# Performance work log

Measured on AMD Instinct MI355X. Metric: run time of the kernel, lower is better.

## Reference

```python
import jax, jax.numpy as jnp
import numpy as np

HIDDEN = 1024
N_HEADS = 16
HEAD_DIM = HIDDEN // N_HEADS  # 64
SCALE = HEAD_DIM ** -0.5
B, QL, KVL = 2, 2048, 4096


def setup_inputs() -> dict:
    key = jax.random.key(0)
    ks = jax.random.split(key, 7)
    s = 0.02
    return {
        "query_states": jax.random.normal(ks[0], (B, QL, HIDDEN), jnp.float32),
        "key_states": jax.random.normal(ks[1], (B, KVL, HIDDEN), jnp.float32),
        "value_states": jax.random.normal(ks[2], (B, KVL, HIDDEN), jnp.float32),
        # torch nn.Linear weights: shape [out, in], applied as x @ W.T
        "Wq": jax.random.normal(ks[3], (HIDDEN, HIDDEN), jnp.float32) * s,
        "Wk": jax.random.normal(ks[4], (HIDDEN, HIDDEN), jnp.float32) * s,
        "Wv": jax.random.normal(ks[5], (HIDDEN, HIDDEN), jnp.float32) * s,
        "Wo": jax.random.normal(ks[6], (HIDDEN, HIDDEN), jnp.float32) * s,
    }


def reference(query_states, key_states, value_states, Wq, Wk, Wv, Wo):
    b, ql, _ = query_states.shape
    kvl = key_states.shape[1]
    # projections (torch Linear: x @ W.T)
    q = query_states @ Wq.T  # [b, ql, H]
    k = key_states @ Wk.T    # [b, kvl, H]
    v = value_states @ Wv.T  # [b, kvl, H]
    # split heads -> [b, h, s, d]
    q = q.reshape(b, ql, N_HEADS, HEAD_DIM).transpose(0, 2, 1, 3)
    k = k.reshape(b, kvl, N_HEADS, HEAD_DIM).transpose(0, 2, 1, 3)
    v = v.reshape(b, kvl, N_HEADS, HEAD_DIM).transpose(0, 2, 1, 3)
    # scores [b, h, ql, kvl]
    scores = jnp.einsum("bhqd,bhkd->bhqk", q, k) * SCALE
    attn = jax.nn.softmax(scores, axis=-1)
    out = jnp.einsum("bhqk,bhkd->bhqd", attn, v)  # [b, h, ql, d]
    out = out.transpose(0, 2, 1, 3).reshape(b, ql, HIDDEN)
    return out @ Wo.T
```

## Files before the change

### kernel.cpp

```cpp
#include <hip/hip_runtime.h>

#define HID   1024
#define NH    16
#define HD    64
#define QL    2048
#define KVL   4096
#define NB    2
#define QSCALE 0.180336880111120426f

typedef short s8v  __attribute__((ext_vector_type(8)));
typedef short s4v  __attribute__((ext_vector_type(4)));
typedef float f4v  __attribute__((ext_vector_type(4)));
typedef float f16x __attribute__((ext_vector_type(16)));

__device__ __forceinline__ unsigned short f2bf(float f) {
  unsigned int u = __builtin_bit_cast(unsigned int, f);
  u += 0x7FFFu + ((u >> 16) & 1u);
  return (unsigned short)(u >> 16);
}
__device__ __forceinline__ float bf2f(unsigned short h) {
  unsigned int u = ((unsigned int)h) << 16;
  return __builtin_bit_cast(float, u);
}
__device__ __forceinline__ float fexp2(float x) {
#if __has_builtin(__builtin_amdgcn_exp2f)
  return __builtin_amdgcn_exp2f(x);
#else
  return exp2f(x);
#endif
}

__device__ __forceinline__ unsigned truncpk(float lo, float hi) {
  unsigned ulo = __builtin_bit_cast(unsigned, lo);
  unsigned uhi = __builtin_bit_cast(unsigned, hi);
  return (ulo >> 16) | (uhi & 0xFFFF0000u);
}

__global__ __launch_bounds__(256)
void cast_all(const float* __restrict__ q, const float* __restrict__ k,
              const float* __restrict__ v, const float* __restrict__ wq,
              const float* __restrict__ wk, const float* __restrict__ wv,
              const float* __restrict__ wo, unsigned short* __restrict__ dst) {
  size_t c = (size_t)blockIdx.x * 256 + threadIdx.x;
  const float* src; size_t lc; float sc = 1.0f;
  if (c < 524288)       { src = q;  lc = c; }
  else if (c < 1572864) { src = k;  lc = c - 524288; }
  else if (c < 2621440) { src = v;  lc = c - 1572864; }
  else if (c < 2752512) { src = wq; lc = c - 2621440; sc = QSCALE; }
  else if (c < 2883584) { src = wk; lc = c - 2752512; }
  else if (c < 3014656) { src = wv; lc = c - 2883584; }
  else                  { src = wo; lc = c - 3014656; }
  const float4* p = (const float4*)(src + lc * 8);
  float4 a = p[0], b = p[1];
  union { s8v v8; unsigned short h[8]; } u;
  u.h[0] = f2bf(a.x * sc); u.h[1] = f2bf(a.y * sc);
  u.h[2] = f2bf(a.z * sc); u.h[3] = f2bf(a.w * sc);
  u.h[4] = f2bf(b.x * sc); u.h[5] = f2bf(b.y * sc);
  u.h[6] = f2bf(b.z * sc); u.h[7] = f2bf(b.w * sc);
  *(s8v*)(dst + c * 8) = u.v8;
}

typedef const __attribute__((address_space(1))) unsigned int* gas_t;
typedef __attribute__((address_space(3))) unsigned int*       las_t;

__device__ __forceinline__ void gl_lds16(const unsigned short* g, unsigned short* l) {
  __builtin_amdgcn_global_load_lds((gas_t)(const void*)g, (las_t)(void*)l, 16, 0, 0);
}

template <bool OUT_BF16>
__device__ __forceinline__ void gemm_body(const unsigned short* __restrict__ A,
                                          const unsigned short* __restrict__ B,
                                          void* __restrict__ Cv, int N, int K,
                                          int bx, int by,
                                          unsigned short (*As)[128 * 32],
                                          unsigned short (*Bs)[128 * 32]) {
  const int tid  = threadIdx.x;
  const int wave = tid >> 6, lane = tid & 63;
  const int wm = wave >> 1, wn = wave & 1;
  const int quad = lane >> 4, l15 = lane & 15;
  const int row0 = by * 128;
  const int col0 = bx * 128;
  const int srow = lane >> 2;
  const int scol = (lane & 3) * 8;

  f4v acc[4][4] = {};

#define G_STAGE(KI, BI)                                                         \
  {                                                                             \
    _Pragma("unroll")                                                           \
    for (int cc = 0; cc < 2; cc++) {                                            \
      int c = wave + cc * 4;                                                    \
      gl_lds16(A + (size_t)(row0 + c * 16 + srow) * K + (KI) * 32 + scol,       \
               &As[BI][c * 512]);                                               \
      gl_lds16(B + (size_t)(col0 + c * 16 + srow) * K + (KI) * 32 + scol,       \
               &Bs[BI][c * 512]);                                               \
    }                                                                           \
  }

  const int nk = K >> 5;
  G_STAGE(0, 0);
  __syncthreads();

  for (int ki = 0; ki < nk; ki++) {
    const int cur = ki & 1;
    if (ki + 1 < nk) G_STAGE(ki + 1, 1 - cur);

    s8v af[4], bf[4];
#pragma unroll
    for (int i = 0; i < 4; i++)
      af[i] = *(const s8v*)&As[cur][(wm * 64 + i * 16 + l15) * 32 + quad * 8];
#pragma unroll
    for (int j = 0; j < 4; j++)
      bf[j] = *(const s8v*)&Bs[cur][(wn * 64 + j * 16 + l15) * 32 + quad * 8];
#pragma unroll
    for (int i = 0; i < 4; i++)
#pragma unroll
      for (int j = 0; j < 4; j++)
        acc[i][j] = __builtin_amdgcn_mfma_f32_16x16x32_bf16(af[i], bf[j],
                                                            acc[i][j], 0, 0, 0);
    __syncthreads();
  }
#undef G_STAGE

#pragma unroll
  for (int i = 0; i < 4; i++) {
#pragma unroll
    for (int j = 0; j < 4; j++) {
      int r = row0 + wm * 64 + i * 16 + quad * 4;
      int c = col0 + wn * 64 + j * 16 + l15;
#pragma unroll
      for (int reg = 0; reg < 4; reg++) {
        float v = acc[i][j][reg];
        if constexpr (OUT_BF16)
          ((unsigned short*)Cv)[(size_t)(r + reg) * N + c] = f2bf(v);
        else
          ((float*)Cv)[(size_t)(r + reg) * N + c] = v;
      }
    }
  }
}

__global__ __launch_bounds__(256, 4)
void proj_fused(const unsigned short* __restrict__ qc, const unsigned short* __restrict__ kc,
                const unsigned short* __restrict__ vc, const unsigned short* __restrict__ wqc,
                const unsigned short* __restrict__ wkc, const unsigned short* __restrict__ wvc,
                unsigned short* __restrict__ qp, unsigned short* __restrict__ kp,
                unsigned short* __restrict__ vpt) {
  __shared__ unsigned short As[2][128 * 32];
  __shared__ unsigned short Bs[2][128 * 32];
  int bid = blockIdx.x;
  if (bid < 256) {
    gemm_body<true>(qc, wqc, qp, HID, HID, bid & 7, bid >> 3, As, Bs);
  } else if (bid < 768) {
    int l = bid - 256;
    gemm_body<true>(kc, wkc, kp, HID, HID, l & 7, l >> 3, As, Bs);
  } else {
    int l = bid - 768;
    int b = l >> 8, r = l & 255;
    gemm_body<true>(wvc, vc + (size_t)b * KVL * HID,
                    vpt + (size_t)b * HID * KVL, KVL, HID, r & 31, r >> 5, As, Bs);
  }
}

__global__ __launch_bounds__(256, 4)
void o_gemm(const unsigned short* __restrict__ ao, const unsigned short* __restrict__ woc,
            float* __restrict__ out) {
  __shared__ unsigned short As[2][128 * 32];
  __shared__ unsigned short Bs[2][128 * 32];
  int bid = blockIdx.x;
  gemm_body<false>(ao, woc, out, HID, HID, bid & 7, bid >> 3, As, Bs);
}

#define LDSK 40

template <typename T>
__device__ __forceinline__ void stage_tile(unsigned short* dst, const T* src,
                                           int ld, int tid, float sc) {
#pragma unroll
  for (int rep = 0; rep < 2; rep++) {
    int s = rep * 256 + tid;
    int row = s >> 2;
    int cs  = (s & 3) * 8;
    const T* p = src + (size_t)row * ld + cs;
    s8v val;
    if constexpr (sizeof(T) == 4) {
      float4 f0 = *(const float4*)p;
      float4 f1 = *(const float4*)(p + 4);
      union { s8v v; unsigned short h[8]; } u;
      u.h[0] = f2bf(f0.x * sc); u.h[1] = f2bf(f0.y * sc);
      u.h[2] = f2bf(f0.z * sc); u.h[3] = f2bf(f0.w * sc);
      u.h[4] = f2bf(f1.x * sc); u.h[5] = f2bf(f1.y * sc);
      u.h[6] = f2bf(f1.z * sc); u.h[7] = f2bf(f1.w * sc);
      val = u.v;
    } else {
      val = *(const s8v*)p;
    }
    *(s8v*)&dst[row * LDSK + cs] = val;
  }
}

template <typename TA, typename TB, bool OUT_BF16>
__global__ __launch_bounds__(256)
void gemm_conv(const TA* __restrict__ A, const TB* __restrict__ B,
               void* __restrict__ Cv, int M, int N, int K, float bscale,
               long long bz, long long cz) {
  __shared__ unsigned short As[128 * LDSK];
  __shared__ unsigned short Bs[128 * LDSK];
  const TB* Bp = B + (size_t)blockIdx.z * (size_t)bz;
  const int tid  = threadIdx.x;
  const int wave = tid >> 6, lane = tid & 63;
  const int wm = wave >> 1, wn = wave & 1;
  const int quad = lane >> 4, l15 = lane & 15;
  const int row0 = blockIdx.y * 128;
  const int col0 = blockIdx.x * 128;

  f4v acc[4][4] = {};

  for (int k0 = 0; k0 < K; k0 += 32) {
    __syncthreads();
    stage_tile(As, A + (size_t)row0 * K + k0, K, tid, 1.0f);
    stage_tile(Bs, Bp + (size_t)col0 * K + k0, K, tid, bscale);
    __syncthreads();

    s8v af[4], bf[4];
#pragma unroll
    for (int i = 0; i < 4; i++)
      af[i] = *(const s8v*)&As[(wm * 64 + i * 16 + l15) * LDSK + quad * 8];
#pragma unroll
    for (int j = 0; j < 4; j++)
      bf[j] = *(const s8v*)&Bs[(wn * 64 + j * 16 + l15) * LDSK + quad * 8];
#pragma unroll
    for (int i = 0; i < 4; i++)
#pragma unroll
      for (int j = 0; j < 4; j++)
        acc[i][j] = __builtin_amdgcn_mfma_f32_16x16x32_bf16(af[i], bf[j],
                                                            acc[i][j], 0, 0, 0);
  }

  char* Cp = (char*)Cv + (size_t)blockIdx.z * (size_t)cz * (OUT_BF16 ? 2 : 4);
#pragma unroll
  for (int i = 0; i < 4; i++) {
#pragma unroll
    for (int j = 0; j < 4; j++) {
      int r = row0 + wm * 64 + i * 16 + quad * 4;
      int c = col0 + wn * 64 + j * 16 + l15;
#pragma unroll
      for (int reg = 0; reg < 4; reg++) {
        float v = acc[i][j][reg];
        if constexpr (OUT_BF16)
          ((unsigned short*)Cp)[(size_t)(r + reg) * N + c] = f2bf(v);
        else
          ((float*)Cp)[(size_t)(r + reg) * N + c] = v;
      }
    }
  }
}

template <bool SPLIT>
__global__ __launch_bounds__(256, 2)
void attn11(const unsigned short* __restrict__ qp,
            const unsigned short* __restrict__ kp,
            const unsigned short* __restrict__ vpt,
            unsigned short* __restrict__ po,
            float* __restrict__ pl,
            unsigned short* __restrict__ ao) {
  __shared__ unsigned short Ks[2][64 * 64];
  __shared__ unsigned short Vt[2][64 * 64];

  const int bid  = blockIdx.x;
  const int qb   = bid & 7;
  const int h    = (bid >> 3) & 15;
  const int b    = (bid >> 7) & 1;
  const int half = SPLIT ? (bid >> 8) : 0;
  const int tid  = threadIdx.x;
  const int wave = tid >> 6, lane = tid & 63;
  const int l31  = lane & 31, hi = lane >> 5;
  const int q0   = qb * 256 + wave * 64;
  const int kvoff = half * (KVL / 2);
  const int NT   = SPLIT ? (KVL / 128) : (KVL / 64);

  const unsigned short* kbase = kp + (size_t)b * KVL * HID + h * HD + (size_t)kvoff * HID;
  const unsigned short* vbase = vpt + (size_t)(b * NH + h) * HD * KVL + kvoff;

  int prow[2], pcol[2], pbase[2];
#pragma unroll
  for (int i = 0; i < 2; i++) {
    int p = (i * 4 + wave) * 64 + lane;
    prow[i]  = p >> 3;
    pcol[i]  = ((p & 7) ^ (prow[i] & 7)) * 8;
    pbase[i] = (i * 4 + wave) * 512;
  }

  s8v qf[2][4];
#pragma unroll
  for (int nt = 0; nt < 2; nt++) {
    const unsigned short* qrow = qp + (size_t)(b * QL + q0 + nt * 32 + l31) * HID + h * HD;
#pragma unroll
    for (int ks = 0; ks < 4; ks++)
      qf[nt][ks] = *(const s8v*)(qrow + ks * 16 + hi * 8);
  }

  union { unsigned w[4]; s8v v; } uones;
#pragma unroll
  for (int i = 0; i < 4; i++) uones.w[i] = 0x3F803F80u;

  f16x oacc[2][2] = {};
  f16x lacc[2]    = {};

#define STAGE_KV(KT, BI)                                                        \
  {                                                                             \
    const unsigned short* kb = kbase + (size_t)((KT) * 64) * HID;               \
    const unsigned short* vb = vbase + (KT) * 64;                               \
    _Pragma("unroll")                                                           \
    for (int i = 0; i < 2; i++) {                                               \
      gl_lds16(kb + (size_t)prow[i] * HID + pcol[i], &Ks[BI][pbase[i]]);        \
      gl_lds16(vb + (size_t)prow[i] * KVL + pcol[i], &Vt[BI][pbase[i]]);        \
    }                                                                           \
  }

  STAGE_KV(0, 0);
  __syncthreads();

  for (int kt = 0; kt < NT; kt++) {
    const int cur = kt & 1;
    if (kt + 1 < NT) STAGE_KV(kt + 1, 1 - cur);

    f16x sacc[2][2] = {};
    __builtin_amdgcn_s_setprio(1);
#pragma unroll
    for (int ks = 0; ks < 4; ks++)
#pragma unroll
      for (int mt = 0; mt < 2; mt++) {
        int row = mt * 32 + l31;
        int xc  = ((ks * 2 + hi) ^ (row & 7)) * 8;
        s8v kf = *(const s8v*)&Ks[cur][row * 64 + xc];
#pragma unroll
        for (int nt = 0; nt < 2; nt++)
          sacc[mt][nt] = __builtin_amdgcn_mfma_f32_32x32x16_bf16(kf, qf[nt][ks],
                                                                 sacc[mt][nt], 0, 0, 0);
      }
    __builtin_amdgcn_s_setprio(0);

    unsigned paw[2][4][4];
#pragma unroll
    for (int nt = 0; nt < 2; nt++) {
#pragma unroll
      for (int mt = 0; mt < 2; mt++) {
        float e[16];
#pragma unroll
        for (int r = 0; r < 16; r++) e[r] = fexp2(sacc[mt][nt][r]);
#pragma unroll
        for (int s = 0; s < 4; s++) {
          paw[nt][s][2 * mt]     = truncpk(e[4 * s],     e[4 * s + 1]);
          paw[nt][s][2 * mt + 1] = truncpk(e[4 * s + 2], e[4 * s + 3]);
        }
      }
    }

    __builtin_amdgcn_s_setprio(1);
#pragma unroll
    for (int s = 0; s < 4; s++) {
      union { unsigned w[4]; s8v v; } up[2];
#pragma unroll
      for (int nt = 0; nt < 2; nt++) {
        up[nt].w[0] = paw[nt][s][0]; up[nt].w[1] = paw[nt][s][1];
        up[nt].w[2] = paw[nt][s][2]; up[nt].w[3] = paw[nt][s][3];
      }
#pragma unroll
      for (int dt = 0; dt < 2; dt++) {
        int row = dt * 32 + l31;
        int o0  = row * 64 + ((s ^ (row & 7)) * 8) + hi * 4;
        union { s4v hh[2]; s8v v; } uv;
        uv.hh[0] = *(const s4v*)&Vt[cur][o0];
        uv.hh[1] = *(const s4v*)&Vt[cur][o0 ^ 32];
#pragma unroll
        for (int nt = 0; nt < 2; nt++)
          oacc[nt][dt] = __builtin_amdgcn_mfma_f32_32x32x16_bf16(up[nt].v, uv.v,
                                                                 oacc[nt][dt], 0, 0, 0);
      }
#pragma unroll
      for (int nt = 0; nt < 2; nt++)
        lacc[nt] = __builtin_amdgcn_mfma_f32_32x32x16_bf16(up[nt].v, uones.v,
                                                           lacc[nt], 0, 0, 0);
    }
    __builtin_amdgcn_s_setprio(0);

    __syncthreads();
  }
#undef STAGE_KV

  if constexpr (SPLIT) {
    unsigned short* pob = po + (size_t)half * NB * QL * HID;
#pragma unroll
    for (int nt = 0; nt < 2; nt++) {
#pragma unroll
      for (int dt = 0; dt < 2; dt++)
#pragma unroll
        for (int r = 0; r < 16; r++) {
          int qq = q0 + nt * 32 + (r & 3) + 8 * (r >> 2) + 4 * hi;
          int cc = h * HD + dt * 32 + l31;
          pob[(size_t)(b * QL + qq) * HID + cc] = f2bf(oacc[nt][dt][r]);
        }
      if (l31 == 0) {
        float* plb = pl + (size_t)half * NB * NH * QL + (size_t)(b * NH + h) * QL;
#pragma unroll
        for (int r = 0; r < 16; r++)
          plb[q0 + nt * 32 + (r & 3) + 8 * (r >> 2) + 4 * hi] = lacc[nt][r];
      }
    }
  } else {
#pragma unroll
    for (int nt = 0; nt < 2; nt++) {
#pragma unroll
      for (int r = 0; r < 16; r++) {
        float lv = 1.0f / lacc[nt][r];
        int qq = q0 + nt * 32 + (r & 3) + 8 * (r >> 2) + 4 * hi;
#pragma unroll
        for (int dt = 0; dt < 2; dt++) {
          int cc = h * HD + dt * 32 + l31;
          ao[(size_t)(b * QL + qq) * HID + cc] = f2bf(oacc[nt][dt][r] * lv);
        }
      }
    }
  }
}

__global__ __launch_bounds__(256)
void combine(const unsigned short* __restrict__ po, const float* __restrict__ pl,
             unsigned short* __restrict__ ao) {
  int t  = blockIdx.x * 256 + threadIdx.x;
  int r  = t >> 7;
  int c8 = t & 127;
  int b = r >> 11, q = r & 2047, h = c8 >> 3;
  size_t lidx = (size_t)(b * NH + h) * QL + q;
  float l = pl[lidx] + pl[(size_t)NB * NH * QL + lidx];
  float inv = 1.0f / l;
  size_t off = (size_t)r * HID + c8 * 8;
  s8v a = *(const s8v*)(po + off);
  s8v c = *(const s8v*)(po + (size_t)NB * QL * HID + off);
  union { s8v v8; unsigned short hh[8]; } ua, uc, uo;
  ua.v8 = a; uc.v8 = c;
#pragma unroll
  for (int e = 0; e < 8; e++)
    uo.hh[e] = f2bf((bf2f(ua.hh[e]) + bf2f(uc.hh[e])) * inv);
  *(s8v*)(ao + off) = uo.v8;
}

extern "C" void kernel_launch(void* const* d_in, const int* in_sizes, int n_in,
                              void* d_out, int out_size, void* d_ws, size_t ws_size,
                              hipStream_t stream) {
  const float* q  = (const float*)d_in[0];
  const float* k  = (const float*)d_in[1];
  const float* v  = (const float*)d_in[2];
  const float* Wq = (const float*)d_in[3];
  const float* Wk = (const float*)d_in[4];
  const float* Wv = (const float*)d_in[5];
  const float* Wo = (const float*)d_in[6];
  float* out = (float*)d_out;
  char* ws = (char*)d_ws;
  dim3 blk(256);

  const long long MB = 1024 * 1024;
  if (ws_size >= (size_t)88 * MB) {
    unsigned short* qc  = (unsigned short*)(ws);
    unsigned short* kc  = (unsigned short*)(ws + 8 * MB);
    unsigned short* vc  = (unsigned short*)(ws + 24 * MB);
    unsigned short* wqc = (unsigned short*)(ws + 40 * MB);
    unsigned short* wkc = (unsigned short*)(ws + 42 * MB);
    unsigned short* wvc = (unsigned short*)(ws + 44 * MB);
    unsigned short* woc = (unsigned short*)(ws + 46 * MB);
    unsigned short* qp  = (unsigned short*)(ws + 48 * MB);
    unsigned short* kp  = (unsigned short*)(ws + 56 * MB);
    unsigned short* vpt = (unsigned short*)(ws + 72 * MB);
    unsigned short* ao  = (unsigned short*)(ws);
    unsigned short* po  = (unsigned short*)(ws + 8 * MB);
    float*          pl  = (float*)(ws + 40 * MB);

    cast_all<<<12288, blk, 0, stream>>>(q, k, v, Wq, Wk, Wv, Wo, (unsigned short*)ws);
    proj_fused<<<1280, blk, 0, stream>>>(qc, kc, vc, wqc, wkc, wvc, qp, kp, vpt);
    attn11<true><<<512, blk, 0, stream>>>(qp, kp, vpt, po, pl, nullptr);
    combine<<<2048, blk, 0, stream>>>(po, pl, ao);
    o_gemm<<<256, blk, 0, stream>>>(ao, woc, out);
  } else {
    unsigned short* qp  = (unsigned short*)(ws);
    unsigned short* kp  = (unsigned short*)(ws + 8 * MB);
    unsigned short* vpt = (unsigned short*)(ws + 24 * MB);
    unsigned short* ao  = (unsigned short*)(ws + 40 * MB);

    gemm_conv<float, float, true><<<dim3(8, 32), blk, 0, stream>>>(q, Wq, qp, NB * QL, HID, HID, QSCALE, 0, 0);
    gemm_conv<float, float, true><<<dim3(8, 64), blk, 0, stream>>>(k, Wk, kp, NB * KVL, HID, HID, 1.0f, 0, 0);
    gemm_conv<float, float, true><<<dim3(32, 8, 2), blk, 0, stream>>>(Wv, v, vpt, HID, KVL, HID, 1.0f,
                                                                      (long long)KVL * HID, (long long)HID * KVL);
    attn11<false><<<256, blk, 0, stream>>>(qp, kp, vpt, nullptr, nullptr, ao);
    gemm_conv<unsigned short, float, false><<<dim3(8, 32), blk, 0, stream>>>(ao, Wo, out, NB * QL, HID, HID, 1.0f, 0, 0);
  }
}
```

Measured before the change: 306.0 us.

## Replace split-KV attention plus combine with smaller-tile full-KV attention kernel

Drops the split-KV attention and its separate combine kernel. Each wave now owns 32 query rows instead of 64, so a block covers 128 queries, and 512 blocks walk the full KV range while writing normalized output directly. The launch bound rises to 4 blocks per CU, and a block-index remap groups the heads of one batch across XCDs for L2 reuse. This removes the partial-output round trip and one kernel launch, but halves MFMA reuse of each K/V tile loaded from LDS and doubles total K/V staging traffic.

```diff
diff --git a/kernel.cpp b/kernel.cpp
--- a/kernel.cpp
+++ b/kernel.cpp
@@ -256,31 +256,26 @@
   }
 }
 
-template <bool SPLIT>
-__global__ __launch_bounds__(256, 2)
-void attn11(const unsigned short* __restrict__ qp,
+__global__ __launch_bounds__(256, 4)
+void attn12(const unsigned short* __restrict__ qp,
             const unsigned short* __restrict__ kp,
             const unsigned short* __restrict__ vpt,
-            unsigned short* __restrict__ po,
-            float* __restrict__ pl,
             unsigned short* __restrict__ ao) {
   __shared__ unsigned short Ks[2][64 * 64];
   __shared__ unsigned short Vt[2][64 * 64];
 
-  const int bid  = blockIdx.x;
-  const int qb   = bid & 7;
-  const int h    = (bid >> 3) & 15;
-  const int b    = (bid >> 7) & 1;
-  const int half = SPLIT ? (bid >> 8) : 0;
+  const int logical = (blockIdx.x & 7) * 64 + (blockIdx.x >> 3);
+  const int qb   = logical & 15;
+  const int h    = (logical >> 4) & 15;
+  const int b    = logical >> 8;
   const int tid  = threadIdx.x;
   const int wave = tid >> 6, lane = tid & 63;
   const int l31  = lane & 31, hi = lane >> 5;
-  const int q0   = qb * 256 + wave * 64;
-  const int kvoff = half * (KVL / 2);
-  const int NT   = SPLIT ? (KVL / 128) : (KVL / 64);
-
-  const unsigned short* kbase = kp + (size_t)b * KVL * HID + h * HD + (size_t)kvoff * HID;
-  const unsigned short* vbase = vpt + (size_t)(b * NH + h) * HD * KVL + kvoff;
+  const int q0   = qb * 128 + wave * 32;
+  const int NT   = KVL / 64;
+
+  const unsigned short* kbase = kp + (size_t)b * KVL * HID + h * HD;
+  const unsigned short* vbase = vpt + (size_t)(b * NH + h) * HD * KVL;
 
   int prow[2], pcol[2], pbase[2];
 #pragma unroll
@@ -291,21 +286,20 @@
     pbase[i] = (i * 4 + wave) * 512;
   }
 
-  s8v qf[2][4];
-#pragma unroll
-  for (int nt = 0; nt < 2; nt++) {
-    const unsigned short* qrow = qp + (size_t)(b * QL + q0 + nt * 32 + l31) * HID + h * HD;
+  s8v qf[4];
+  {
+    const unsigned short* qrow = qp + (size_t)(b * QL + q0 + l31) * HID + h * HD;
 #pragma unroll
     for (int ks = 0; ks < 4; ks++)
-      qf[nt][ks] = *(const s8v*)(qrow + ks * 16 + hi * 8);
+      qf[ks] = *(const s8v*)(qrow + ks * 16 + hi * 8);
   }
 
   union { unsigned w[4]; s8v v; } uones;
 #pragma unroll
   for (int i = 0; i < 4; i++) uones.w[i] = 0x3F803F80u;
 
-  f16x oacc[2][2] = {};
-  f16x lacc[2]    = {};
+  f16x oacc[2] = {};
+  f16x lacc    = {};
 
 #define STAGE_KV(KT, BI)                                                        \
   {                                                                             \
@@ -325,7 +319,7 @@
     const int cur = kt & 1;
     if (kt + 1 < NT) STAGE_KV(kt + 1, 1 - cur);
 
-    f16x sacc[2][2] = {};
+    f16x sacc[2] = {};
     __builtin_amdgcn_s_setprio(1);
 #pragma unroll
     for (int ks = 0; ks < 4; ks++)
@@ -334,38 +328,30 @@
         int row = mt * 32 + l31;
         int xc  = ((ks * 2 + hi) ^ (row & 7)) * 8;
         s8v kf = *(const s8v*)&Ks[cur][row * 64 + xc];
-#pragma unroll
-        for (int nt = 0; nt < 2; nt++)
-          sacc[mt][nt] = __builtin_amdgcn_mfma_f32_32x32x16_bf16(kf, qf[nt][ks],
-                                                                 sacc[mt][nt], 0, 0, 0);
+        sacc[mt] = __builtin_amdgcn_mfma_f32_32x32x16_bf16(kf, qf[ks],
+                                                           sacc[mt], 0, 0, 0);
       }
     __builtin_amdgcn_s_setprio(0);
 
-    unsigned paw[2][4][4];
-#pragma unroll
-    for (int nt = 0; nt < 2; nt++) {
-#pragma unroll
-      for (int mt = 0; mt < 2; mt++) {
-        float e[16];
-#pragma unroll
-        for (int r = 0; r < 16; r++) e[r] = fexp2(sacc[mt][nt][r]);
-#pragma unroll
-        for (int s = 0; s < 4; s++) {
-          paw[nt][s][2 * mt]     = truncpk(e[4 * s],     e[4 * s + 1]);
-          paw[nt][s][2 * mt + 1] = truncpk(e[4 * s + 2], e[4 * s + 3]);
-        }
+    unsigned paw[4][4];
+#pragma unroll
+    for (int mt = 0; mt < 2; mt++) {
+      float e[16];
+#pragma unroll
+      for (int r = 0; r < 16; r++) e[r] = fexp2(sacc[mt][r]);
+#pragma unroll
+      for (int s = 0; s < 4; s++) {
+        paw[s][2 * mt]     = truncpk(e[4 * s],     e[4 * s + 1]);
+        paw[s][2 * mt + 1] = truncpk(e[4 * s + 2], e[4 * s + 3]);
       }
     }
 
     __builtin_amdgcn_s_setprio(1);
 #pragma unroll
     for (int s = 0; s < 4; s++) {
-      union { unsigned w[4]; s8v v; } up[2];
-#pragma unroll
-      for (int nt = 0; nt < 2; nt++) {
-        up[nt].w[0] = paw[nt][s][0]; up[nt].w[1] = paw[nt][s][1];
-        up[nt].w[2] = paw[nt][s][2]; up[nt].w[3] = paw[nt][s][3];
-      }
+      union { unsigned w[4]; s8v v; } up;
+      up.w[0] = paw[s][0]; up.w[1] = paw[s][1];
+      up.w[2] = paw[s][2]; up.w[3] = paw[s][3];
 #pragma unroll
       for (int dt = 0; dt < 2; dt++) {
         int row = dt * 32 + l31;
@@ -373,15 +359,11 @@
         union { s4v hh[2]; s8v v; } uv;
         uv.hh[0] = *(const s4v*)&Vt[cur][o0];
         uv.hh[1] = *(const s4v*)&Vt[cur][o0 ^ 32];
-#pragma unroll
-        for (int nt = 0; nt < 2; nt++)
-          oacc[nt][dt] = __builtin_amdgcn_mfma_f32_32x32x16_bf16(up[nt].v, uv.v,
-                                                                 oacc[nt][dt], 0, 0, 0);
+        oacc[dt] = __builtin_amdgcn_mfma_f32_32x32x16_bf16(up.v, uv.v,
+                                                           oacc[dt], 0, 0, 0);
       }
-#pragma unroll
-      for (int nt = 0; nt < 2; nt++)
-        lacc[nt] = __builtin_amdgcn_mfma_f32_32x32x16_bf16(up[nt].v, uones.v,
-                                                           lacc[nt], 0, 0, 0);
+      lacc = __builtin_amdgcn_mfma_f32_32x32x16_bf16(up.v, uones.v,
+                                                     lacc, 0, 0, 0);
     }
     __builtin_amdgcn_s_setprio(0);
 
@@ -389,61 +371,16 @@
   }
 #undef STAGE_KV
 
-  if constexpr (SPLIT) {
-    unsigned short* pob = po + (size_t)half * NB * QL * HID;
-#pragma unroll
-    for (int nt = 0; nt < 2; nt++) {
-#pragma unroll
-      for (int dt = 0; dt < 2; dt++)
-#pragma unroll
-        for (int r = 0; r < 16; r++) {
-          int qq = q0 + nt * 32 + (r & 3) + 8 * (r >> 2) + 4 * hi;
-          int cc = h * HD + dt * 32 + l31;
-          pob[(size_t)(b * QL + qq) * HID + cc] = f2bf(oacc[nt][dt][r]);
-        }
-      if (l31 == 0) {
-        float* plb = pl + (size_t)half * NB * NH * QL + (size_t)(b * NH + h) * QL;
-#pragma unroll
-        for (int r = 0; r < 16; r++)
-          plb[q0 + nt * 32 + (r & 3) + 8 * (r >> 2) + 4 * hi] = lacc[nt][r];
-      }
-    }
-  } else {
-#pragma unroll
-    for (int nt = 0; nt < 2; nt++) {
-#pragma unroll
-      for (int r = 0; r < 16; r++) {
-        float lv = 1.0f / lacc[nt][r];
-        int qq = q0 + nt * 32 + (r & 3) + 8 * (r >> 2) + 4 * hi;
-#pragma unroll
-        for (int dt = 0; dt < 2; dt++) {
-          int cc = h * HD + dt * 32 + l31;
-          ao[(size_t)(b * QL + qq) * HID + cc] = f2bf(oacc[nt][dt][r] * lv);
-        }
-      }
-    }
-  }
-}
-
-__global__ __launch_bounds__(256)
-void combine(const unsigned short* __restrict__ po, const float* __restrict__ pl,
-             unsigned short* __restrict__ ao) {
-  int t  = blockIdx.x * 256 + threadIdx.x;
-  int r  = t >> 7;
-  int c8 = t & 127;
-  int b = r >> 11, q = r & 2047, h = c8 >> 3;
-  size_t lidx = (size_t)(b * NH + h) * QL + q;
-  float l = pl[lidx] + pl[(size_t)NB * NH * QL + lidx];
-  float inv = 1.0f / l;
-  size_t off = (size_t)r * HID + c8 * 8;
-  s8v a = *(const s8v*)(po + off);
-  s8v c = *(const s8v*)(po + (size_t)NB * QL * HID + off);
-  union { s8v v8; unsigned short hh[8]; } ua, uc, uo;
-  ua.v8 = a; uc.v8 = c;
-#pragma unroll
-  for (int e = 0; e < 8; e++)
-    uo.hh[e] = f2bf((bf2f(ua.hh[e]) + bf2f(uc.hh[e])) * inv);
-  *(s8v*)(ao + off) = uo.v8;
+#pragma unroll
+  for (int r = 0; r < 16; r++) {
+    float lv = 1.0f / lacc[r];
+    int qq = q0 + (r & 3) + 8 * (r >> 2) + 4 * hi;
+#pragma unroll
+    for (int dt = 0; dt < 2; dt++) {
+      int cc = h * HD + dt * 32 + l31;
+      ao[(size_t)(b * QL + qq) * HID + cc] = f2bf(oacc[dt][r] * lv);
+    }
+  }
 }
 
 extern "C" void kernel_launch(void* const* d_in, const int* in_sizes, int n_in,
@@ -473,13 +410,10 @@
     unsigned short* kp  = (unsigned short*)(ws + 56 * MB);
     unsigned short* vpt = (unsigned short*)(ws + 72 * MB);
     unsigned short* ao  = (unsigned short*)(ws);
-    unsigned short* po  = (unsigned short*)(ws + 8 * MB);
-    float*          pl  = (float*)(ws + 40 * MB);
 
     cast_all<<<12288, blk, 0, stream>>>(q, k, v, Wq, Wk, Wv, Wo, (unsigned short*)ws);
     proj_fused<<<1280, blk, 0, stream>>>(qc, kc, vc, wqc, wkc, wvc, qp, kp, vpt);
-    attn11<true><<<512, blk, 0, stream>>>(qp, kp, vpt, po, pl, nullptr);
-    combine<<<2048, blk, 0, stream>>>(po, pl, ao);
+    attn12<<<512, blk, 0, stream>>>(qp, kp, vpt, ao);
     o_gemm<<<256, blk, 0, stream>>>(ao, woc, out);
   } else {
     unsigned short* qp  = (unsigned short*)(ws);
@@ -491,7 +425,7 @@
     gemm_conv<float, float, true><<<dim3(8, 64), blk, 0, stream>>>(k, Wk, kp, NB * KVL, HID, HID, 1.0f, 0, 0);
     gemm_conv<float, float, true><<<dim3(32, 8, 2), blk, 0, stream>>>(Wv, v, vpt, HID, KVL, HID, 1.0f,
                                                                       (long long)KVL * HID, (long long)HID * KVL);
-    attn11<false><<<256, blk, 0, stream>>>(qp, kp, vpt, nullptr, nullptr, ao);
+    attn12<<<512, blk, 0, stream>>>(qp, kp, vpt, ao);
     gemm_conv<unsigned short, float, false><<<dim3(8, 32), blk, 0, stream>>>(ao, Wo, out, NB * QL, HID, HID, 1.0f, 0, 0);
   }
 }
```

Measured after the change: 331.7 us. 8.4% more time.
